# Performance work log

Hardware: AMD Instinct MI355X
Metric: run time of the kernel (lower is better)

## Reference

```python
import jax, jax.numpy as jnp
import numpy as np
import math

B, L, D, H = 4, 1024, 512, 8
TAU = 0.1
LN_EPS = 1e-5


def _attn(xq, xk, xv, wq, bq, wk, bk, wv, bv, wo, bo, energy=None, threshold=None):
    Bq, Lq, Dm = xq.shape
    Dh = Dm // H
    Q = (xq @ wq.T + bq).reshape(Bq, Lq, H, Dh)
    K = (xk @ wk.T + bk).reshape(Bq, -1, H, Dh)
    V = (xv @ wv.T + bv).reshape(Bq, -1, H, Dh)
    sc = jnp.einsum('bqhd,bkhd->bhqk', Q, K) / jnp.sqrt(jnp.float32(Dh))
    if energy is not None:
        # mask keys whose mean |energy| over channels is below threshold
        mask = jnp.abs(energy).mean(-1)[:, None, None, :] > threshold  # (B,1,1,Lk)
        sc = jnp.where(mask, sc, -jnp.inf)
    w = jnp.nan_to_num(jax.nn.softmax(sc, axis=-1))  # nan->0 for fully-masked rows
    o = jnp.einsum('bhqk,bkhd->bqhd', w, V).reshape(Bq, Lq, Dm)
    return o @ wo.T + bo


def _ln(x, w, b):
    m = x.mean(-1, keepdims=True)
    v = x.var(-1, keepdims=True)
    return (x - m) / jnp.sqrt(v + LN_EPS) * w + b


def _mlp(x, w1, b1, w2, b2):
    h = jax.nn.gelu(x @ w1.T + b1, approximate=False)  # torch nn.GELU default = exact
    return h @ w2.T + b2


def setup_inputs():
    key = jax.random.key(0)
    ks = list(jax.random.split(key, 64))

    def nxt():
        return ks.pop(0)

    def w(shape, scale=0.02):
        return jax.random.normal(nxt(), shape, dtype=jnp.float32) * scale

    inp = {
        'LL': jax.random.normal(nxt(), (B, D, L), dtype=jnp.float32),
        'LH': jax.random.normal(nxt(), (B, D, L), dtype=jnp.float32),
        'raw_tau': jnp.float32(math.log(TAU / (1.0 - TAU))),
    }
    for p in ('llA', 'lhA', 'crA'):
        for nm in ('q', 'k', 'v', 'o'):
            inp[f'{p}_w{nm}'] = w((D, D))
            inp[f'{p}_b{nm}'] = jnp.zeros((D,), jnp.float32)
    for p in ('mlp_ll', 'mlp_lh'):
        inp[f'{p}_w1'] = w((4 * D, D))
        inp[f'{p}_b1'] = jnp.zeros((4 * D,), jnp.float32)
        inp[f'{p}_w2'] = w((D, 4 * D))
        inp[f'{p}_b2'] = jnp.zeros((D,), jnp.float32)
    inp['n1_w'] = jnp.ones((D,), jnp.float32)
    inp['n1_b'] = jnp.zeros((D,), jnp.float32)
    inp['n2_w'] = jnp.ones((D,), jnp.float32)
    inp['n2_b'] = jnp.zeros((D,), jnp.float32)
    return inp


def reference(LL, LH, raw_tau,
              llA_wq, llA_bq, llA_wk, llA_bk, llA_wv, llA_bv, llA_wo, llA_bo,
              lhA_wq, lhA_bq, lhA_wk, lhA_bk, lhA_wv, lhA_bv, lhA_wo, lhA_bo,
              crA_wq, crA_bq, crA_wk, crA_bk, crA_wv, crA_bv, crA_wo, crA_bo,
              mlp_ll_w1, mlp_ll_b1, mlp_ll_w2, mlp_ll_b2,
              mlp_lh_w1, mlp_lh_b1, mlp_lh_w2, mlp_lh_b2,
              n1_w, n1_b, n2_w, n2_b):
    tau = jax.nn.sigmoid(raw_tau)
    ll_s = jnp.transpose(LL, (0, 2, 1))  # (B,L,D)
    lh_s = jnp.transpose(LH, (0, 2, 1))
    ll_o = _attn(ll_s, ll_s, ll_s, llA_wq, llA_bq, llA_wk, llA_bk, llA_wv, llA_bv, llA_wo, llA_bo)
    lh_o = _attn(lh_s, lh_s, lh_s, lhA_wq, lhA_bq, lhA_wk, lhA_bk, lhA_wv, lhA_bv, lhA_wo, lhA_bo,
                 energy=lh_s, threshold=tau)
    cr_o = _attn(ll_o, lh_o, lh_o, crA_wq, crA_bq, crA_wk, crA_bk, crA_wv, crA_bv, crA_wo, crA_bo)
    ll_f = _ln(ll_s + ll_o + cr_o, n1_w, n1_b)
    ll_f = _mlp(ll_f, mlp_ll_w1, mlp_ll_b1, mlp_ll_w2, mlp_ll_b2) + ll_f
    lh_f = _ln(lh_s + lh_o, n2_w, n2_b)
    lh_f = _mlp(lh_f, mlp_lh_w1, mlp_lh_b1, mlp_lh_w2, mlp_lh_b2) + lh_f
    return (jnp.transpose(ll_f, (0, 2, 1)), jnp.transpose(lh_f, (0, 2, 1)))
```

## Files before the change

kernel.cpp:

```cpp
#include <hip/hip_runtime.h>
#include <hip/hip_bf16.h>
#include <stdint.h>

typedef unsigned short u16;
typedef __bf16 bf16_t;
typedef bf16_t bf16x8 __attribute__((ext_vector_type(8)));
typedef float f32x4 __attribute__((ext_vector_type(4)));

#define DEV static __device__ __forceinline__

DEV u16 f2b(float f) {
    __hip_bfloat16 h = __float2bfloat16(f);
    return __builtin_bit_cast(u16, h);
}

DEV bf16x8 ld_frag(const u16* p) {
    uint4 u = *reinterpret_cast<const uint4*>(p);
    return __builtin_bit_cast(bf16x8, u);
}

DEV float gelu(float v) {
    float y = 0.79788456080286536f * (v + 0.044715f * v * v * v);
    float e = __expf(-2.f * fabsf(y));
    float th = (1.f - e) / (1.f + e);
    th = copysignf(th, y);
    return 0.5f * v * (1.f + th);
}

DEV void gl_lds16(const u16* g, u16* l) {
    __builtin_amdgcn_global_load_lds(
        (const __attribute__((address_space(1))) void*)(uintptr_t)g,
        (__attribute__((address_space(3))) void*)(unsigned int)(uintptr_t)l,
        16, 0, 0);
}

struct ConvEnt { const float* s; u16* d; int n; };
struct ConvArgs { ConvEnt e[16]; };

__global__ __launch_bounds__(256) void k_conv(ConvArgs a) {
    const ConvEnt en = a.e[blockIdx.y];
    for (int i = (blockIdx.x * 256 + threadIdx.x) * 4; i < en.n; i += 256 * 256 * 4) {
        const float4 f = *reinterpret_cast<const float4*>(en.s + i);
        unsigned r0 = (unsigned)f2b(f.x) | ((unsigned)f2b(f.y) << 16);
        unsigned r1 = (unsigned)f2b(f.z) | ((unsigned)f2b(f.w) << 16);
        uint2 rr; rr.x = r0; rr.y = r1;
        *reinterpret_cast<uint2*>(en.d + i) = rr;
    }
}

struct CpyEnt { const float* s; float* d; };
struct CpyArgs { CpyEnt e[8]; };

__global__ __launch_bounds__(256) void k_cpyf(CpyArgs a) {
    const CpyEnt en = a.e[blockIdx.y];
    int i = blockIdx.x * 256 + threadIdx.x;
    en.d[i] = en.s[i];
}

__global__ __launch_bounds__(256) void k_tin(const float* __restrict__ LL, const float* __restrict__ LH,
                                             float* __restrict__ llf, u16* __restrict__ llb,
                                             float* __restrict__ lhf, u16* __restrict__ lhb) {
    __shared__ float t[32][33];
    int z = blockIdx.z, b = z & 3;
    const float* in = (z < 4) ? LL : LH;
    float* of = (z < 4) ? llf : lhf;
    u16* ob = (z < 4) ? llb : lhb;
    int l0 = blockIdx.x * 32, d0 = blockIdx.y * 32;
    int tx = threadIdx.x, ty = threadIdx.y;
#pragma unroll
    for (int j = 0; j < 4; ++j) {
        int d = d0 + ty + j * 8;
        t[ty + j * 8][tx] = in[((size_t)b * 512 + d) * 1024 + l0 + tx];
    }
    __syncthreads();
#pragma unroll
    for (int j = 0; j < 4; ++j) {
        int l = l0 + ty + j * 8;
        float v = t[tx][ty + j * 8];
        size_t o = ((size_t)b * 1024 + l) * 512 + d0 + tx;
        of[o] = v;
        ob[o] = f2b(v);
    }
}

__global__ __launch_bounds__(256) void k_tout(const float* __restrict__ y0, const float* __restrict__ y1,
                                              float* __restrict__ out) {
    __shared__ float t[32][33];
    int z = blockIdx.z, b = z & 3;
    const float* in = (z < 4) ? y0 : y1;
    float* o = out + ((z < 4) ? 0 : (size_t)4096 * 512);
    int l0 = blockIdx.x * 32, d0 = blockIdx.y * 32;
    int tx = threadIdx.x, ty = threadIdx.y;
#pragma unroll
    for (int j = 0; j < 4; ++j) {
        int l = l0 + ty + j * 8;
        t[ty + j * 8][tx] = in[((size_t)b * 1024 + l) * 512 + d0 + tx];
    }
    __syncthreads();
#pragma unroll
    for (int j = 0; j < 4; ++j) {
        int d = d0 + ty + j * 8;
        o[((size_t)b * 512 + d) * 1024 + l0 + tx] = t[tx][ty + j * 8];
    }
}

__global__ __launch_bounds__(256) void k_mask(const float* __restrict__ lh_s,
                                              const float* __restrict__ raw_tau,
                                              float* __restrict__ kbias) {
    int row = blockIdx.x * 4 + (threadIdx.x >> 6);
    int lane = threadIdx.x & 63;
    const float* p = lh_s + (size_t)row * 512 + lane * 8;
    float s = 0.f;
#pragma unroll
    for (int j = 0; j < 8; ++j) s += fabsf(p[j]);
#pragma unroll
    for (int m = 32; m >= 1; m >>= 1) s += __shfl_xor(s, m, 64);
    float tau = 1.f / (1.f + expf(-raw_tau[0]));
    if (lane == 0) kbias[row] = (s * (1.f / 512.f) > tau) ? 0.f : -3.0e38f;
}

__global__ __launch_bounds__(256) void k_ln(const float* __restrict__ a, const float* __restrict__ b,
                                            const float* __restrict__ c, const float* __restrict__ w,
                                            const float* __restrict__ bi,
                                            float* __restrict__ of, u16* __restrict__ ob) {
    int row = blockIdx.x * 4 + (threadIdx.x >> 6);
    int lane = threadIdx.x & 63;
    size_t base = (size_t)row * 512 + lane * 8;
    float x[8];
#pragma unroll
    for (int j = 0; j < 8; ++j) {
        float v = a[base + j] + b[base + j];
        if (c) v += c[base + j];
        x[j] = v;
    }
    float s = 0.f, s2 = 0.f;
#pragma unroll
    for (int j = 0; j < 8; ++j) { s += x[j]; s2 += x[j] * x[j]; }
#pragma unroll
    for (int m = 32; m >= 1; m >>= 1) { s += __shfl_xor(s, m, 64); s2 += __shfl_xor(s2, m, 64); }
    float mean = s * (1.f / 512.f);
    float var = s2 * (1.f / 512.f) - mean * mean;
    float rs = rsqrtf(var + 1e-5f);
#pragma unroll
    for (int j = 0; j < 8; ++j) {
        float y = (x[j] - mean) * rs * w[lane * 8 + j] + bi[lane * 8 + j];
        of[base + j] = y;
        ob[base + j] = f2b(y);
    }
}

template <int BM, int BN, int GELU_ACT, int OUTF, int OUTB, int RES, int PACK>
__global__ __launch_bounds__(256) void k_gemm(const u16* __restrict__ A, const u16* __restrict__ W,
                                              const float* __restrict__ bias,
                                              const float* __restrict__ res,
                                              float* __restrict__ Cf, u16* __restrict__ Cb,
                                              u16* __restrict__ Qp, u16* __restrict__ Kp,
                                              u16* __restrict__ Vt, int kB, int vB,
                                              int M, int N, int K, int nwg) {
    constexpr int BK = 64;
    __shared__ alignas(16) u16 Al[2][BM * BK];
    __shared__ alignas(16) u16 Wl[2][BN * BK];
    int bid;
    {
        const int orig = blockIdx.x;
        const int xcd = orig & 7, lin = orig >> 3;
        const int q = nwg >> 3, r = nwg & 7;
        bid = (xcd < r ? xcd * (q + 1) : r * (q + 1) + (xcd - r) * q) + lin;
    }
    const int nny = N / BN;
    const int m0 = (bid / nny) * BM, n0 = (bid % nny) * BN;

    const int t = threadIdx.x, w = t >> 6, l = t & 63;
    constexpr int FM = BM / 32, FN = BN / 32;
    const int wr = w >> 1, wc = w & 1;
    const int lq = l & 15, lg = l >> 4;
    f32x4 acc[FM][FN] = {};

    const int srow = l >> 3, schunk = l & 7;
    auto stage = [&](int kcol, int buf) {
#pragma unroll
        for (int i = 0; i < BM / 32; ++i) {
            const int row = i * 32 + w * 8 + srow;
            gl_lds16(A + (size_t)(m0 + row) * K + kcol + ((schunk ^ (row & 7)) * 8),
                     &Al[buf][(i * 32 + w * 8) * BK]);
        }
#pragma unroll
        for (int i = 0; i < BN / 32; ++i) {
            const int row = i * 32 + w * 8 + srow;
            gl_lds16(W + (size_t)(n0 + row) * K + kcol + ((schunk ^ (row & 7)) * 8),
                     &Wl[buf][(i * 32 + w * 8) * BK]);
        }
    };

    stage(0, 0);
    const int KT = K / BK;
    for (int kt = 0; kt < KT; ++kt) {
        const int cur = kt & 1;
        __syncthreads();
        if (kt + 1 < KT) stage((kt + 1) * BK, cur ^ 1);
#pragma unroll
        for (int s = 0; s < 2; ++s) {
            bf16x8 af[FM], bw[FN];
#pragma unroll
            for (int i = 0; i < FM; ++i) {
                const int row = wr * (BM / 2) + i * 16 + lq;
                af[i] = ld_frag(&Al[cur][row * BK + (((s * 4 + lg) ^ (row & 7)) * 8)]);
            }
#pragma unroll
            for (int j = 0; j < FN; ++j) {
                const int row = wc * (BN / 2) + j * 16 + lq;
                bw[j] = ld_frag(&Wl[cur][row * BK + (((s * 4 + lg) ^ (row & 7)) * 8)]);
            }
#pragma unroll
            for (int i = 0; i < FM; ++i)
#pragma unroll
                for (int j = 0; j < FN; ++j)
                    acc[i][j] = __builtin_amdgcn_mfma_f32_16x16x32_bf16(af[i], bw[j], acc[i][j], 0, 0, 0);
        }
    }

    if (PACK && n0 >= vB) {
        u16* T = (u16*)Al;
        constexpr int CH = BM / 8, CMASK = CH - 1, SH = (CH == 16) ? 4 : 3;
        __syncthreads();
#pragma unroll
        for (int i = 0; i < FM; ++i) {
#pragma unroll
            for (int j = 0; j < FN; ++j) {
                const int ni = wc * (BN / 2) + j * 16 + lq;
                const float bn = bias[n0 + ni];
#pragma unroll
                for (int r2 = 0; r2 < 4; ++r2) {
                    const int mi = wr * (BM / 2) + i * 16 + lg * 4 + r2;
                    T[ni * BM + (((mi >> 3) ^ (ni & CMASK)) * 8) + (mi & 7)] = f2b(acc[i][j][r2] + bn);
                }
            }
        }
        __syncthreads();
        const int bb = m0 >> 10, mloc = m0 & 1023;
        const int mc = t & CMASK, nib = t >> SH;
        constexpr int RPP = 256 / CH;
#pragma unroll
        for (int p2 = 0; p2 < BN / RPP; ++p2) {
            const int ni = nib + p2 * RPP;
            uint4 u = *reinterpret_cast<const uint4*>(&T[ni * BM + ((mc ^ (ni & CMASK)) * 8)]);
            const int d = n0 - vB + ni;
            *reinterpret_cast<uint4*>(
                &Vt[((size_t)(bb * 8 + (d >> 6)) * 64 + (d & 63)) * 1024 + mloc + mc * 8]) = u;
        }
        return;
    }

#pragma unroll
    for (int i = 0; i < FM; ++i) {
#pragma unroll
        for (int j = 0; j < FN; ++j) {
            const int n = n0 + wc * (BN / 2) + j * 16 + lq;
            const float bn = bias[n];
#pragma unroll
            for (int r2 = 0; r2 < 4; ++r2) {
                const int m = m0 + wr * (BM / 2) + i * 16 + lg * 4 + r2;
                float v = acc[i][j][r2] + bn;
                if (GELU_ACT) v = gelu(v);
                if (PACK) {
                    const int bb = m >> 10, ll_ = m & 1023;
                    if (n >= kB) {
                        const int d = n - kB;
                        Kp[((size_t)(bb * 8 + (d >> 6)) * 1024 + ll_) * 64 + (d & 63)] = f2b(v);
                    } else {
                        Qp[((size_t)(bb * 8 + (n >> 6)) * 1024 + ll_) * 64 + (n & 63)] = f2b(v * 0.125f);
                    }
                } else {
                    size_t o = (size_t)m * N + n;
                    if (RES) v += res[o];
                    if (OUTF) Cf[o] = v;
                    if (OUTB) Cb[o] = f2b(v);
                }
            }
        }
    }
}

__global__ __launch_bounds__(256) void k_attn(const u16* __restrict__ Qp, const u16* __restrict__ Kp,
                                              const u16* __restrict__ Vtp, u16* __restrict__ O,
                                              const float* __restrict__ kbias) {
    constexpr int L = 1024;
    __shared__ alignas(16) u16 Kl[2][64 * 64];
    __shared__ alignas(16) u16 Vl[2][64 * 64];
    __shared__ alignas(16) u16 Pl[64 * 72];
    const int t = threadIdx.x, w = t >> 6, l = t & 63;
    const int q0 = blockIdx.x * 64;
    const int h = blockIdx.y, bz = blockIdx.z, bh = bz * 8 + h;
    const int lq = l & 15, lg = l >> 4;
    const float* kb = (kbias != nullptr && bz >= 4) ? (kbias + (size_t)(bz - 4) * L) : nullptr;

    bf16x8 qa0, qa1;
    {
        const u16* qp = Qp + ((size_t)bh * L + q0 + w * 16 + lq) * 64 + lg * 8;
        qa0 = ld_frag(qp);
        qa1 = ld_frag(qp + 32);
    }

    const int r0 = w * 16 + (l >> 3), r1 = r0 + 8, c = l & 7;
    const u16* Ksrc0 = Kp + (size_t)bh * L * 64 + (size_t)r0 * 64 + ((c ^ (r0 & 7)) * 8);
    const u16* Ksrc1 = Kp + (size_t)bh * L * 64 + (size_t)r1 * 64 + ((c ^ (r1 & 7)) * 8);
    const u16* Vsrc0 = Vtp + (size_t)bh * 64 * L + (size_t)r0 * L + ((c ^ (r0 & 7)) * 8);
    const u16* Vsrc1 = Vtp + (size_t)bh * 64 * L + (size_t)r1 * L + ((c ^ (r1 & 7)) * 8);

    auto stage = [&](int k0, int buf) {
        gl_lds16(Ksrc0 + (size_t)k0 * 64, &Kl[buf][(w * 16) * 64]);
        gl_lds16(Ksrc1 + (size_t)k0 * 64, &Kl[buf][(w * 16 + 8) * 64]);
        gl_lds16(Vsrc0 + k0, &Vl[buf][(w * 16) * 64]);
        gl_lds16(Vsrc1 + k0, &Vl[buf][(w * 16 + 8) * 64]);
    };

    int addrA[4][2];
#pragma unroll
    for (int f = 0; f < 4; ++f) {
        int row = f * 16 + lq;
#pragma unroll
        for (int s = 0; s < 2; ++s) addrA[f][s] = row * 64 + (((s * 4 + lg) ^ (row & 7)) * 8);
    }
    const int paddr0 = (w * 16 + lq) * 72 + lg * 8;

    f32x4 oacc[4] = {};
    float lrow[4] = {0.f, 0.f, 0.f, 0.f};

    stage(0, 0);
    for (int kt = 0; kt < 16; ++kt) {
        const int cur = kt & 1;
        __syncthreads();
        if (kt + 1 < 16) stage((kt + 1) * 64, cur ^ 1);

        f32x4 sc4[4];
#pragma unroll
        for (int f = 0; f < 4; ++f) {
            f32x4 a = {};
            a = __builtin_amdgcn_mfma_f32_16x16x32_bf16(qa0, ld_frag(&Kl[cur][addrA[f][0]]), a, 0, 0, 0);
            a = __builtin_amdgcn_mfma_f32_16x16x32_bf16(qa1, ld_frag(&Kl[cur][addrA[f][1]]), a, 0, 0, 0);
            sc4[f] = a;
        }
#pragma unroll
        for (int f = 0; f < 4; ++f) {
            float bv = kb ? kb[kt * 64 + f * 16 + lq] : 0.f;
#pragma unroll
            for (int r = 0; r < 4; ++r) {
                float pv = __expf(sc4[f][r] + bv);
                lrow[r] += pv;
                Pl[(w * 16 + lg * 4 + r) * 72 + f * 16 + lq] = f2b(pv);
            }
        }
        bf16x8 pa0 = ld_frag(&Pl[paddr0]);
        bf16x8 pa1 = ld_frag(&Pl[paddr0 + 32]);
#pragma unroll
        for (int db = 0; db < 4; ++db) {
            oacc[db] = __builtin_amdgcn_mfma_f32_16x16x32_bf16(pa0, ld_frag(&Vl[cur][addrA[db][0]]), oacc[db], 0, 0, 0);
            oacc[db] = __builtin_amdgcn_mfma_f32_16x16x32_bf16(pa1, ld_frag(&Vl[cur][addrA[db][1]]), oacc[db], 0, 0, 0);
        }
    }
#pragma unroll
    for (int r = 0; r < 4; ++r) {
        float v = lrow[r];
#pragma unroll
        for (int msk = 8; msk >= 1; msk >>= 1) v += __shfl_xor(v, msk, 16);
        lrow[r] = v;
    }
#pragma unroll
    for (int db = 0; db < 4; ++db) {
#pragma unroll
        for (int r = 0; r < 4; ++r) {
            float denom = lrow[r];
            float v = (denom > 0.f) ? oacc[db][r] / denom : 0.f;
            O[((size_t)bz * L + q0 + w * 16 + lg * 4 + r) * 512 + h * 64 + db * 16 + lq] = f2b(v);
        }
    }
}

extern "C" void kernel_launch(void* const* d_in, const int* in_sizes, int n_in,
                              void* d_out, int out_size, void* d_ws, size_t ws_size,
                              hipStream_t stream) {
    const int M = 4096, D = 512, DFF = 2048, Hz = 8;
    const float* LL = (const float*)d_in[0];
    const float* LH = (const float*)d_in[1];
    const float* raw_tau = (const float*)d_in[2];
    auto F = [&](int i) { return (const float*)d_in[i]; };
    const int BIG = 1 << 28;

    char* p = (char*)d_ws;
    auto alloc = [&](size_t bytes) { void* r = (void*)p; p += (bytes + 255) & ~(size_t)255; return r; };
    const size_t MDf = (size_t)M * D * 4, MDb = (size_t)M * D * 2;
    float* ll_s_f = (float*)alloc(MDf);
    float* lh_s_f = (float*)alloc(MDf);
    u16* ll_s_b = (u16*)alloc(MDb);
    u16* lh_s_b = (u16*)alloc(MDb);
    u16* Qp = (u16*)alloc(2 * MDb);
    u16* Kp = (u16*)alloc(2 * MDb);
    u16* Vt = (u16*)alloc(2 * MDb);
    u16* Cxb = (u16*)alloc(2 * MDb);
    float* ll_o_f = (float*)alloc(MDf);
    u16* ll_o_b = (u16*)alloc(MDb);
    float* lh_o_f = (float*)alloc(MDf);
    u16* lh_o_b = (u16*)alloc(MDb);
    float* cr_o_f = (float*)alloc(MDf);
    float* ln_f_ll = (float*)alloc(MDf);
    float* ln_f_lh = (float*)alloc(MDf);
    u16* ln_b = (u16*)alloc(MDb);
    u16* hb = (u16*)alloc((size_t)M * DFF * 2);
    float* yf_ll = (float*)alloc(MDf);
    float* yf_lh = (float*)alloc(MDf);
    float* kbias = (float*)alloc(4096 * 4);
    float* bqkv_ll = (float*)alloc(1536 * 4);
    float* bqkv_lh = (float*)alloc(1536 * 4);
    float* bkv_cr = (float*)alloc(1024 * 4);
    const size_t WDD = (size_t)262144;
    u16* wqkv_ll = (u16*)alloc(3 * WDD * 2);
    u16* wqkv_lh = (u16*)alloc(3 * WDD * 2);
    u16* wkv_cr = (u16*)alloc(2 * WDD * 2);
    u16* wq_cr = (u16*)alloc(WDD * 2);
    u16* wo_ll = (u16*)alloc(WDD * 2);
    u16* wo_lh = (u16*)alloc(WDD * 2);
    u16* wo_cr = (u16*)alloc(WDD * 2);
    u16* wm[4];
    for (int i = 0; i < 4; ++i) wm[i] = (u16*)alloc((size_t)1048576 * 2);

    const size_t SET = (size_t)4 * 8 * 1024 * 64;

    ConvArgs ca;
    ca.e[0] = {F(3), wqkv_ll, (int)WDD};
    ca.e[1] = {F(5), wqkv_ll + WDD, (int)WDD};
    ca.e[2] = {F(7), wqkv_ll + 2 * WDD, (int)WDD};
    ca.e[3] = {F(11), wqkv_lh, (int)WDD};
    ca.e[4] = {F(13), wqkv_lh + WDD, (int)WDD};
    ca.e[5] = {F(15), wqkv_lh + 2 * WDD, (int)WDD};
    ca.e[6] = {F(19), wq_cr, (int)WDD};
    ca.e[7] = {F(21), wkv_cr, (int)WDD};
    ca.e[8] = {F(23), wkv_cr + WDD, (int)WDD};
    ca.e[9] = {F(9), wo_ll, (int)WDD};
    ca.e[10] = {F(17), wo_lh, (int)WDD};
    ca.e[11] = {F(25), wo_cr, (int)WDD};
    ca.e[12] = {F(27), wm[0], 1048576};
    ca.e[13] = {F(29), wm[1], 1048576};
    ca.e[14] = {F(31), wm[2], 1048576};
    ca.e[15] = {F(33), wm[3], 1048576};
    k_conv<<<dim3(256, 16), 256, 0, stream>>>(ca);

    CpyArgs cp;
    cp.e[0] = {F(4), bqkv_ll};
    cp.e[1] = {F(6), bqkv_ll + 512};
    cp.e[2] = {F(8), bqkv_ll + 1024};
    cp.e[3] = {F(12), bqkv_lh};
    cp.e[4] = {F(14), bqkv_lh + 512};
    cp.e[5] = {F(16), bqkv_lh + 1024};
    cp.e[6] = {F(22), bkv_cr};
    cp.e[7] = {F(24), bkv_cr + 512};
    k_cpyf<<<dim3(2, 8), 256, 0, stream>>>(cp);

    k_tin<<<dim3(32, 16, 8), dim3(32, 8), 0, stream>>>(LL, LH, ll_s_f, ll_s_b, lh_s_f, lh_s_b);
    k_mask<<<dim3(1024), 256, 0, stream>>>(lh_s_f, raw_tau, kbias);

    k_gemm<128, 128, 0, 0, 0, 0, 1><<<dim3(384), 256, 0, stream>>>(
        ll_s_b, wqkv_ll, bqkv_ll, nullptr, nullptr, nullptr, Qp, Kp, Vt, 512, 1024, M, 1536, 512, 384);
    k_gemm<128, 128, 0, 0, 0, 0, 1><<<dim3(384), 256, 0, stream>>>(
        lh_s_b, wqkv_lh, bqkv_lh, nullptr, nullptr, nullptr, Qp + SET, Kp + SET, Vt + SET, 512, 1024, M, 1536, 512, 384);
    k_attn<<<dim3(16, 8, 8), 256, 0, stream>>>(Qp, Kp, Vt, Cxb, kbias);
    k_gemm<64, 64, 0, 1, 1, 0, 0><<<dim3(512), 256, 0, stream>>>(
        Cxb, wo_ll, F(10), nullptr, ll_o_f, ll_o_b, nullptr, nullptr, nullptr, 0, BIG, M, 512, 512, 512);
    k_gemm<64, 64, 0, 1, 1, 0, 0><<<dim3(512), 256, 0, stream>>>(
        Cxb + SET, wo_lh, F(18), nullptr, lh_o_f, lh_o_b, nullptr, nullptr, nullptr, 0, BIG, M, 512, 512, 512);
    k_ln<<<dim3(1024), 256, 0, stream>>>(lh_s_f, lh_o_f, nullptr, F(37), F(38), ln_f_lh, ln_b);
    k_gemm<128, 128, 1, 0, 1, 0, 0><<<dim3(512), 256, 0, stream>>>(
        ln_b, wm[2], F(32), nullptr, nullptr, hb, nullptr, nullptr, nullptr, 0, BIG, M, 2048, 512, 512);
    k_gemm<64, 64, 0, 0, 0, 0, 1><<<dim3(512), 256, 0, stream>>>(
        ll_o_b, wq_cr, F(20), nullptr, nullptr, nullptr, Qp, Kp, Vt, BIG, BIG, M, 512, 512, 512);
    k_gemm<64, 64, 0, 0, 0, 0, 1><<<dim3(1024), 256, 0, stream>>>(
        lh_o_b, wkv_cr, bkv_cr, nullptr, nullptr, nullptr, Qp, Kp, Vt, 0, 512, M, 1024, 512, 1024);
    k_attn<<<dim3(16, 8, 4), 256, 0, stream>>>(Qp, Kp, Vt, Cxb, nullptr);
    k_gemm<64, 64, 0, 1, 0, 0, 0><<<dim3(512), 256, 0, stream>>>(
        Cxb, wo_cr, F(26), nullptr, cr_o_f, nullptr, nullptr, nullptr, nullptr, 0, BIG, M, 512, 512, 512);
    k_gemm<64, 64, 0, 1, 0, 1, 0><<<dim3(512), 256, 0, stream>>>(
        hb, wm[3], F(34), ln_f_lh, yf_lh, nullptr, nullptr, nullptr, nullptr, 0, BIG, M, 512, 2048, 512);
    k_ln<<<dim3(1024), 256, 0, stream>>>(ll_s_f, ll_o_f, cr_o_f, F(35), F(36), ln_f_ll, ln_b);
    k_gemm<128, 128, 1, 0, 1, 0, 0><<<dim3(512), 256, 0, stream>>>(
        ln_b, wm[0], F(28), nullptr, nullptr, hb, nullptr, nullptr, nullptr, 0, BIG, M, 2048, 512, 512);
    k_gemm<64, 64, 0, 1, 0, 1, 0><<<dim3(512), 256, 0, stream>>>(
        hb, wm[1], F(30), ln_f_ll, yf_ll, nullptr, nullptr, nullptr, nullptr, 0, BIG, M, 512, 2048, 512);
    k_tout<<<dim3(32, 16, 8), dim3(32, 8), 0, stream>>>(yf_ll, yf_lh, (float*)d_out);
}
```

Before: 277.9 us.

## Batch independent GEMMs into grouped launches, swizzle attention P tile and blocks

After: 273.9 us. Within noise of the previous version (-1.4%).

```diff
diff --git a/kernel.cpp b/kernel.cpp
--- a/kernel.cpp
+++ b/kernel.cpp
@@ -149,24 +149,27 @@
     }
 }
 
-template <int BM, int BN, int GELU_ACT, int OUTF, int OUTB, int RES, int PACK>
-__global__ __launch_bounds__(256) void k_gemm(const u16* __restrict__ A, const u16* __restrict__ W,
-                                              const float* __restrict__ bias,
-                                              const float* __restrict__ res,
-                                              float* __restrict__ Cf, u16* __restrict__ Cb,
-                                              u16* __restrict__ Qp, u16* __restrict__ Kp,
-                                              u16* __restrict__ Vt, int kB, int vB,
-                                              int M, int N, int K, int nwg) {
+struct GP {
+    const u16* A; const u16* W; const float* bias; const float* res;
+    float* Cf; u16* Cb; u16* Qp; u16* Kp; u16* Vt;
+    int N, K, kB, vB, nwg;
+};
+
+template <int BM, int BN, int GELU_ACT, int PACK>
+__global__ __launch_bounds__(256) void k_gemm(GP p0, GP p1, int M) {
     constexpr int BK = 64;
     __shared__ alignas(16) u16 Al[2][BM * BK];
     __shared__ alignas(16) u16 Wl[2][BN * BK];
+    GP g = (blockIdx.y == 0) ? p0 : p1;
+    const int orig = blockIdx.x;
+    if (orig >= g.nwg) return;
     int bid;
     {
-        const int orig = blockIdx.x;
         const int xcd = orig & 7, lin = orig >> 3;
-        const int q = nwg >> 3, r = nwg & 7;
+        const int q = g.nwg >> 3, r = g.nwg & 7;
         bid = (xcd < r ? xcd * (q + 1) : r * (q + 1) + (xcd - r) * q) + lin;
     }
+    const int K = g.K, N = g.N;
     const int nny = N / BN;
     const int m0 = (bid / nny) * BM, n0 = (bid % nny) * BN;
 
@@ -181,13 +184,13 @@
 #pragma unroll
         for (int i = 0; i < BM / 32; ++i) {
             const int row = i * 32 + w * 8 + srow;
-            gl_lds16(A + (size_t)(m0 + row) * K + kcol + ((schunk ^ (row & 7)) * 8),
+            gl_lds16(g.A + (size_t)(m0 + row) * K + kcol + ((schunk ^ (row & 7)) * 8),
                      &Al[buf][(i * 32 + w * 8) * BK]);
         }
 #pragma unroll
         for (int i = 0; i < BN / 32; ++i) {
             const int row = i * 32 + w * 8 + srow;
-            gl_lds16(W + (size_t)(n0 + row) * K + kcol + ((schunk ^ (row & 7)) * 8),
+            gl_lds16(g.W + (size_t)(n0 + row) * K + kcol + ((schunk ^ (row & 7)) * 8),
                      &Wl[buf][(i * 32 + w * 8) * BK]);
         }
     };
@@ -219,7 +222,7 @@
         }
     }
 
-    if (PACK && n0 >= vB) {
+    if (PACK && n0 >= g.vB) {
         u16* T = (u16*)Al;
         constexpr int CH = BM / 8, CMASK = CH - 1, SH = (CH == 16) ? 4 : 3;
         __syncthreads();
@@ -228,7 +231,7 @@
 #pragma unroll
             for (int j = 0; j < FN; ++j) {
                 const int ni = wc * (BN / 2) + j * 16 + lq;
-                const float bn = bias[n0 + ni];
+                const float bn = g.bias[n0 + ni];
 #pragma unroll
                 for (int r2 = 0; r2 < 4; ++r2) {
                     const int mi = wr * (BM / 2) + i * 16 + lg * 4 + r2;
@@ -244,9 +247,9 @@
         for (int p2 = 0; p2 < BN / RPP; ++p2) {
             const int ni = nib + p2 * RPP;
             uint4 u = *reinterpret_cast<const uint4*>(&T[ni * BM + ((mc ^ (ni & CMASK)) * 8)]);
-            const int d = n0 - vB + ni;
+            const int d = n0 - g.vB + ni;
             *reinterpret_cast<uint4*>(
-                &Vt[((size_t)(bb * 8 + (d >> 6)) * 64 + (d & 63)) * 1024 + mloc + mc * 8]) = u;
+                &g.Vt[((size_t)(bb * 8 + (d >> 6)) * 64 + (d & 63)) * 1024 + mloc + mc * 8]) = u;
         }
         return;
     }
@@ -256,7 +259,7 @@
 #pragma unroll
         for (int j = 0; j < FN; ++j) {
             const int n = n0 + wc * (BN / 2) + j * 16 + lq;
-            const float bn = bias[n];
+            const float bn = g.bias[n];
 #pragma unroll
             for (int r2 = 0; r2 < 4; ++r2) {
                 const int m = m0 + wr * (BM / 2) + i * 16 + lg * 4 + r2;
@@ -264,17 +267,17 @@
                 if (GELU_ACT) v = gelu(v);
                 if (PACK) {
                     const int bb = m >> 10, ll_ = m & 1023;
-                    if (n >= kB) {
-                        const int d = n - kB;
-                        Kp[((size_t)(bb * 8 + (d >> 6)) * 1024 + ll_) * 64 + (d & 63)] = f2b(v);
+                    if (n >= g.kB) {
+                        const int d = n - g.kB;
+                        g.Kp[((size_t)(bb * 8 + (d >> 6)) * 1024 + ll_) * 64 + (d & 63)] = f2b(v);
                     } else {
-                        Qp[((size_t)(bb * 8 + (n >> 6)) * 1024 + ll_) * 64 + (n & 63)] = f2b(v * 0.125f);
+                        g.Qp[((size_t)(bb * 8 + (n >> 6)) * 1024 + ll_) * 64 + (n & 63)] = f2b(v * 0.125f);
                     }
                 } else {
                     size_t o = (size_t)m * N + n;
-                    if (RES) v += res[o];
-                    if (OUTF) Cf[o] = v;
-                    if (OUTB) Cb[o] = f2b(v);
+                    if (g.res) v += g.res[o];
+                    if (g.Cf) g.Cf[o] = v;
+                    if (g.Cb) g.Cb[o] = f2b(v);
                 }
             }
         }
@@ -283,14 +286,19 @@
 
 __global__ __launch_bounds__(256) void k_attn(const u16* __restrict__ Qp, const u16* __restrict__ Kp,
                                               const u16* __restrict__ Vtp, u16* __restrict__ O,
-                                              const float* __restrict__ kbias) {
+                                              const float* __restrict__ kbias, int nwg) {
     constexpr int L = 1024;
     __shared__ alignas(16) u16 Kl[2][64 * 64];
     __shared__ alignas(16) u16 Vl[2][64 * 64];
-    __shared__ alignas(16) u16 Pl[64 * 72];
+    __shared__ alignas(16) u16 Pl[64 * 64];
     const int t = threadIdx.x, w = t >> 6, l = t & 63;
-    const int q0 = blockIdx.x * 64;
-    const int h = blockIdx.y, bz = blockIdx.z, bh = bz * 8 + h;
+    int bid;
+    {
+        const int orig = blockIdx.x;
+        bid = (orig & 7) * (nwg >> 3) + (orig >> 3);
+    }
+    const int bh = bid >> 4, q0 = (bid & 15) * 64;
+    const int bz = bh >> 3, h = bh & 7;
     const int lq = l & 15, lg = l >> 4;
     const float* kb = (kbias != nullptr && bz >= 4) ? (kbias + (size_t)(bz - 4) * L) : nullptr;
 
@@ -321,7 +329,8 @@
 #pragma unroll
         for (int s = 0; s < 2; ++s) addrA[f][s] = row * 64 + (((s * 4 + lg) ^ (row & 7)) * 8);
     }
-    const int paddr0 = (w * 16 + lq) * 72 + lg * 8;
+    const int paddr0 = (w * 16 + lq) * 64 + ((lg ^ (lq & 7)) * 8);
+    const int paddr1 = (w * 16 + lq) * 64 + (((4 + lg) ^ (lq & 7)) * 8);
 
     f32x4 oacc[4] = {};
     float lrow[4] = {0.f, 0.f, 0.f, 0.f};
@@ -347,11 +356,12 @@
             for (int r = 0; r < 4; ++r) {
                 float pv = __expf(sc4[f][r] + bv);
                 lrow[r] += pv;
-                Pl[(w * 16 + lg * 4 + r) * 72 + f * 16 + lq] = f2b(pv);
+                const int prow = w * 16 + lg * 4 + r;
+                Pl[prow * 64 + (((f * 2 + (lq >> 3)) ^ (prow & 7)) * 8) + (lq & 7)] = f2b(pv);
             }
         }
         bf16x8 pa0 = ld_frag(&Pl[paddr0]);
-        bf16x8 pa1 = ld_frag(&Pl[paddr0 + 32]);
+        bf16x8 pa1 = ld_frag(&Pl[paddr1]);
 #pragma unroll
         for (int db = 0; db < 4; ++db) {
             oacc[db] = __builtin_amdgcn_mfma_f32_16x16x32_bf16(pa0, ld_frag(&Vl[cur][addrA[db][0]]), oacc[db], 0, 0, 0);
@@ -379,7 +389,7 @@
 extern "C" void kernel_launch(void* const* d_in, const int* in_sizes, int n_in,
                               void* d_out, int out_size, void* d_ws, size_t ws_size,
                               hipStream_t stream) {
-    const int M = 4096, D = 512, DFF = 2048, Hz = 8;
+    const int M = 4096;
     const float* LL = (const float*)d_in[0];
     const float* LH = (const float*)d_in[1];
     const float* raw_tau = (const float*)d_in[2];
@@ -388,7 +398,7 @@
 
     char* p = (char*)d_ws;
     auto alloc = [&](size_t bytes) { void* r = (void*)p; p += (bytes + 255) & ~(size_t)255; return r; };
-    const size_t MDf = (size_t)M * D * 4, MDb = (size_t)M * D * 2;
+    const size_t MDf = (size_t)M * 512 * 4, MDb = (size_t)M * 512 * 2;
     float* ll_s_f = (float*)alloc(MDf);
     float* lh_s_f = (float*)alloc(MDf);
     u16* ll_s_b = (u16*)alloc(MDb);
@@ -405,7 +415,7 @@
     float* ln_f_ll = (float*)alloc(MDf);
     float* ln_f_lh = (float*)alloc(MDf);
     u16* ln_b = (u16*)alloc(MDb);
-    u16* hb = (u16*)alloc((size_t)M * DFF * 2);
+    u16* hb = (u16*)alloc((size_t)M * 2048 * 2);
     float* yf_ll = (float*)alloc(MDf);
     float* yf_lh = (float*)alloc(MDf);
     float* kbias = (float*)alloc(4096 * 4);
@@ -458,31 +468,59 @@
     k_tin<<<dim3(32, 16, 8), dim3(32, 8), 0, stream>>>(LL, LH, ll_s_f, ll_s_b, lh_s_f, lh_s_b);
     k_mask<<<dim3(1024), 256, 0, stream>>>(lh_s_f, raw_tau, kbias);
 
-    k_gemm<128, 128, 0, 0, 0, 0, 1><<<dim3(384), 256, 0, stream>>>(
-        ll_s_b, wqkv_ll, bqkv_ll, nullptr, nullptr, nullptr, Qp, Kp, Vt, 512, 1024, M, 1536, 512, 384);
-    k_gemm<128, 128, 0, 0, 0, 0, 1><<<dim3(384), 256, 0, stream>>>(
-        lh_s_b, wqkv_lh, bqkv_lh, nullptr, nullptr, nullptr, Qp + SET, Kp + SET, Vt + SET, 512, 1024, M, 1536, 512, 384);
-    k_attn<<<dim3(16, 8, 8), 256, 0, stream>>>(Qp, Kp, Vt, Cxb, kbias);
-    k_gemm<64, 64, 0, 1, 1, 0, 0><<<dim3(512), 256, 0, stream>>>(
-        Cxb, wo_ll, F(10), nullptr, ll_o_f, ll_o_b, nullptr, nullptr, nullptr, 0, BIG, M, 512, 512, 512);
-    k_gemm<64, 64, 0, 1, 1, 0, 0><<<dim3(512), 256, 0, stream>>>(
-        Cxb + SET, wo_lh, F(18), nullptr, lh_o_f, lh_o_b, nullptr, nullptr, nullptr, 0, BIG, M, 512, 512, 512);
+    auto gp = [&](const u16* A, const u16* W, const float* bias, int N, int K, int nwg) {
+        GP g = {};
+        g.A = A; g.W = W; g.bias = bias; g.N = N; g.K = K; g.nwg = nwg;
+        g.kB = BIG; g.vB = BIG;
+        return g;
+    };
+
+    {
+        GP a = gp(ll_s_b, wqkv_ll, bqkv_ll, 1536, 512, 384);
+        a.kB = 512; a.vB = 1024; a.Qp = Qp; a.Kp = Kp; a.Vt = Vt;
+        GP b = gp(lh_s_b, wqkv_lh, bqkv_lh, 1536, 512, 384);
+        b.kB = 512; b.vB = 1024; b.Qp = Qp + SET; b.Kp = Kp + SET; b.Vt = Vt + SET;
+        k_gemm<128, 128, 0, 1><<<dim3(384, 2), 256, 0, stream>>>(a, b, M);
+    }
+    k_attn<<<dim3(1024), 256, 0, stream>>>(Qp, Kp, Vt, Cxb, kbias, 1024);
+    {
+        GP a = gp(Cxb, wo_ll, F(10), 512, 512, 512);
+        a.Cf = ll_o_f; a.Cb = ll_o_b;
+        GP b = gp(Cxb + SET, wo_lh, F(18), 512, 512, 512);
+        b.Cf = lh_o_f; b.Cb = lh_o_b;
+        k_gemm<64, 64, 0, 0><<<dim3(512, 2), 256, 0, stream>>>(a, b, M);
+    }
     k_ln<<<dim3(1024), 256, 0, stream>>>(lh_s_f, lh_o_f, nullptr, F(37), F(38), ln_f_lh, ln_b);
-    k_gemm<128, 128, 1, 0, 1, 0, 0><<<dim3(512), 256, 0, stream>>>(
-        ln_b, wm[2], F(32), nullptr, nullptr, hb, nullptr, nullptr, nullptr, 0, BIG, M, 2048, 512, 512);
-    k_gemm<64, 64, 0, 0, 0, 0, 1><<<dim3(512), 256, 0, stream>>>(
-        ll_o_b, wq_cr, F(20), nullptr, nullptr, nullptr, Qp, Kp, Vt, BIG, BIG, M, 512, 512, 512);
-    k_gemm<64, 64, 0, 0, 0, 0, 1><<<dim3(1024), 256, 0, stream>>>(
-        lh_o_b, wkv_cr, bkv_cr, nullptr, nullptr, nullptr, Qp, Kp, Vt, 0, 512, M, 1024, 512, 1024);
-    k_attn<<<dim3(16, 8, 4), 256, 0, stream>>>(Qp, Kp, Vt, Cxb, nullptr);
-    k_gemm<64, 64, 0, 1, 0, 0, 0><<<dim3(512), 256, 0, stream>>>(
-        Cxb, wo_cr, F(26), nullptr, cr_o_f, nullptr, nullptr, nullptr, nullptr, 0, BIG, M, 512, 512, 512);
-    k_gemm<64, 64, 0, 1, 0, 1, 0><<<dim3(512), 256, 0, stream>>>(
-        hb, wm[3], F(34), ln_f_lh, yf_lh, nullptr, nullptr, nullptr, nullptr, 0, BIG, M, 512, 2048, 512);
+    {
+        GP a = gp(ln_b, wm[2], F(32), 2048, 512, 512);
+        a.Cb = hb;
+        k_gemm<128, 128, 1, 0><<<dim3(512, 1), 256, 0, stream>>>(a, a, M);
+    }
+    {
+        GP a = gp(ll_o_b, wq_cr, F(20), 512, 512, 512);
+        a.Qp = Qp;
+        GP b = gp(lh_o_b, wkv_cr, bkv_cr, 1024, 512, 1024);
+        b.kB = 0; b.vB = 512; b.Kp = Kp; b.Vt = Vt;
+        k_gemm<64, 64, 0, 1><<<dim3(1024, 2), 256, 0, stream>>>(a, b, M);
+    }
+    k_attn<<<dim3(512), 256, 0, stream>>>(Qp, Kp, Vt, Cxb, nullptr, 512);
+    {
+        GP a = gp(Cxb, wo_cr, F(26), 512, 512, 512);
+        a.Cf = cr_o_f;
+        GP b = gp(hb, wm[3], F(34), 512, 2048, 512);
+        b.Cf = yf_lh; b.res = ln_f_lh;
+        k_gemm<64, 64, 0, 0><<<dim3(512, 2), 256, 0, stream>>>(a, b, M);
+    }
     k_ln<<<dim3(1024), 256, 0, stream>>>(ll_s_f, ll_o_f, cr_o_f, F(35), F(36), ln_f_ll, ln_b);
-    k_gemm<128, 128, 1, 0, 1, 0, 0><<<dim3(512), 256, 0, stream>>>(
-        ln_b, wm[0], F(28), nullptr, nullptr, hb, nullptr, nullptr, nullptr, 0, BIG, M, 2048, 512, 512);
-    k_gemm<64, 64, 0, 1, 0, 1, 0><<<dim3(512), 256, 0, stream>>>(
-        hb, wm[1], F(30), ln_f_ll, yf_ll, nullptr, nullptr, nullptr, nullptr, 0, BIG, M, 512, 2048, 512);
+    {
+        GP a = gp(ln_b, wm[0], F(28), 2048, 512, 512);
+        a.Cb = hb;
+        k_gemm<128, 128, 1, 0><<<dim3(512, 1), 256, 0, stream>>>(a, a, M);
+    }
+    {
+        GP a = gp(hb, wm[1], F(30), 512, 2048, 512);
+        a.Cf = yf_ll; a.res = ln_f_ll;
+        k_gemm<64, 64, 0, 0><<<dim3(512, 1), 256, 0, stream>>>(a, a, M);
+    }
     k_tout<<<dim3(32, 16, 8), dim3(32, 8), 0, stream>>>(yf_ll, yf_lh, (float*)d_out);
 }
```
